# Optimization experiments

Hardware: AMD Instinct MI355X
Metric: run time of the kernel (lower is better)

Reference implementation:

```python
import jax, jax.numpy as jnp
import numpy as np

N = 200000   # graph nodes
C = 1000     # virtual nodes (clusters)
D = 256      # feature dim (in = hidden = out for this layer)


def setup_inputs() -> dict:
    key = jax.random.key(0)
    ks = jax.random.split(key, 24)
    W = lambda k, shape: jax.random.normal(k, shape, dtype=jnp.float32) * 0.05
    inp = {
        "h": jax.random.normal(ks[0], (N, D), dtype=jnp.float32),
        "g": jax.random.normal(ks[1], (C, D), dtype=jnp.float32),
        "g_hat": jax.random.normal(ks[2], (C, D), dtype=jnp.float32),
        "node2cluster": jax.random.randint(ks[3], (N,), 0, C),
        # AdditiveAttention params (all hidden_dim=D)
        "Wq": W(ks[4], (D, D)),          # query_proj (no bias)
        "Wk": W(ks[5], (D, D)),          # key_proj (no bias)
        "b_attn": jax.random.uniform(ks[6], (D,), jnp.float32, -0.1, 0.1),
        "w_score": W(ks[7], (D,)),       # score_proj weight (D -> 1)
        "b_score": jnp.zeros((), jnp.float32),
        # VNTransmitterUnit.W (D -> D), activation tanh
        "Wv": W(ks[8], (D, D)), "bv": jnp.zeros((D,), jnp.float32),
        # GNTransmitterUnit.F_super (D -> D), tanh
        "Ws": W(ks[9], (D, D)), "bs": jnp.zeros((D,), jnp.float32),
        # gn_merge WarpGateUnit (graph-node side)
        "H1w": W(ks[10], (D, D)), "H1b": jnp.zeros((D,), jnp.float32),
        "G1w": W(ks[11], (D, D)), "G1b": jnp.zeros((D,), jnp.float32),
        # vn_merge WarpGateUnit (virtual-node side)
        "H2w": W(ks[12], (D, D)), "H2b": jnp.zeros((D,), jnp.float32),
        "G2w": W(ks[13], (D, D)), "G2b": jnp.zeros((D,), jnp.float32),
    }
    return inp


def reference(h, g, g_hat, node2cluster,
              Wq, Wk, b_attn, w_score, b_score, Wv, bv, Ws, bs,
              H1w, H1b, G1w, G1b, H2w, H2b, G2w, G2b):
    seg = node2cluster  # (N,) cluster id of each node (the code's vn_index partition)

    # ---- VNTransmitterUnit: segmented additive (Bahdanau) attention, graph -> virtual ----
    # score_proj(tanh(key_proj(cluster_h) + query_proj(g[c]) + bias))
    q = g @ Wq                                             # (C, D)
    k = h @ Wk                                             # (N, D)
    s = jnp.tanh(k + q[seg] + b_attn) @ w_score + b_score  # (N,) per-node score
    # online per-cluster softmax (replaces Python loop over clusters)
    m = jax.ops.segment_max(s, seg, num_segments=C)        # (C,)
    e = jnp.exp(s - m[seg])                                # (N,)
    denom = jax.ops.segment_sum(e, seg, num_segments=C)    # (C,)
    attn = e / denom[seg]                                  # (N,)
    ctx = jax.ops.segment_sum(attn[:, None] * h, seg, num_segments=C)  # (C, D)
    g_trans = jnp.tanh(ctx @ Wv + bv)                      # VNTransmitter: W + tanh

    # ---- GNTransmitterUnit: virtual -> graph, tanh(F_super(g)) then per-node gather ----
    h_trans = jnp.tanh(g @ Ws + bs)                        # (C, D)
    h_trans_n = h_trans[seg]                               # (N, D) index_select by vn_indices[:,1]

    # ---- gn_merge WarpGateUnit: gated fuse on graph nodes ----
    z1 = jax.nn.sigmoid(h @ H1w + H1b + h_trans_n @ G1w + G1b)  # (N, D)
    h_merged = (1.0 - z1) * h + z1 * h_trans_n                   # (N, D)

    # ---- vn_merge WarpGateUnit: gated fuse on virtual nodes (g_hat = vn_update conv out) ----
    z2 = jax.nn.sigmoid(g_trans @ H2w + H2b + g_hat @ G2w + G2b)  # (C, D)
    vx_new = (1.0 - z2) * g_trans + z2 * g_hat                    # (C, D)

    # concat node-side and virtual-side outputs along rows -> (N + C, D)
    return jnp.concatenate([h_merged, vx_new], axis=0)
```

## Files before the change

kernel.cpp:

```cpp
#include <hip/hip_runtime.h>
#include <hip/hip_bf16.h>

#define Nn 200000
#define Cc 1000
#define Dd 256
#define PAD 16
#define NCH8 3125
#define CAP 512

typedef float f32x16 __attribute__((ext_vector_type(16)));
typedef short bf16x8 __attribute__((ext_vector_type(8)));
typedef _Float16 f16x2 __attribute__((ext_vector_type(2)));

#define LOG2E  1.4426950408889634f
#define LOG2E2 2.8853900817779268f

__device__ __forceinline__ unsigned int f2bf(float x){
    union { float f; unsigned int u; } c; c.f = x;
    unsigned int u = c.u;
    u += 0x7fffu + ((u >> 16) & 1u);
    return u >> 16;
}
__device__ __forceinline__ float bf2f(unsigned short b){
    union { unsigned int u; float f; } c; c.u = ((unsigned int)b) << 16;
    return c.f;
}
__device__ __forceinline__ float rcp_(float x){ return __builtin_amdgcn_rcpf(x); }

__global__ void k_prep(const float* __restrict__ Wk, const float* __restrict__ H1w,
                       unsigned short* __restrict__ wfragK, unsigned short* __restrict__ wfragH,
                       int* __restrict__ cnt){
    int t = blockIdx.x*256 + threadIdx.x;
    if (t < Cc*PAD) cnt[t] = 0;
    int arr = t >> 13;
    int s   = t & 8191;
    int ct  = s >> 10;
    int kk  = (s >> 6) & 15;
    int l   = s & 63;
    int col = ct*32 + (l & 31);
    int k0  = kk*16 + (l >> 5)*8;
    const float* W = arr ? H1w : Wk;
    unsigned short* dst = (arr ? wfragH : wfragK) + (size_t)s*8;
    #pragma unroll
    for (int e = 0; e < 8; ++e) dst[e] = (unsigned short)f2bf(W[(size_t)(k0+e)*Dd + col]);
}

__global__ __launch_bounds__(512)
void k_cluster_prep(const float* __restrict__ g, const float* __restrict__ Wq,
                    const float* __restrict__ b_attn,
                    const float* __restrict__ Ws, const float* __restrict__ bs,
                    const float* __restrict__ G1w, const float* __restrict__ G1b,
                    const float* __restrict__ H1b,
                    float* __restrict__ qb, unsigned int* __restrict__ ctht){
    int c = blockIdx.x, t = threadIdx.x;
    int d = t & 255, half = t >> 8;
    __shared__ float gL[Dd], htL[Dd];
    __shared__ float redA[2][Dd], redS[2][Dd];
    if (half == 0) gL[d] = g[(size_t)c*Dd + d];
    __syncthreads();
    int k0 = half*128;
    float aq = 0.f, as = 0.f;
    #pragma unroll 4
    for (int k2 = 0; k2 < 128; ++k2){
        int k = k0 + k2;
        float gv = gL[k];
        aq = fmaf(gv, Wq[k*Dd + d], aq);
        as = fmaf(gv, Ws[k*Dd + d], as);
    }
    redA[half][d] = aq;
    redS[half][d] = as;
    __syncthreads();
    if (half == 0){
        qb[(size_t)c*Dd + d] = redA[0][d] + redA[1][d] + b_attn[d];
        htL[d] = tanhf(redS[0][d] + redS[1][d] + bs[d]);
    }
    __syncthreads();
    float ac = 0.f;
    #pragma unroll 4
    for (int k2 = 0; k2 < 128; ++k2){
        int k = k0 + k2;
        ac = fmaf(htL[k], G1w[k*Dd + d], ac);
    }
    redA[half][d] = ac;
    __syncthreads();
    if (half == 0){
        float acv = redA[0][d] + redA[1][d] + H1b[d] + G1b[d];
        ctht[(size_t)c*Dd + d] = (f2bf(acv) << 16) | f2bf(htL[d]);
    }
}

__global__ void k_scatter(const int* __restrict__ seg, int* __restrict__ cnt, int* __restrict__ order){
    int i = blockIdx.x*256 + threadIdx.x;
    if (i < Nn){
        int c = seg[i];
        int p = atomicAdd(&cnt[c*PAD], 1);
        if (p < CAP) order[c*CAP + p] = i;
    }
}

__global__ __launch_bounds__(1024, 4)
void k_gemm8(const float* __restrict__ h, const unsigned short* __restrict__ wfrag,
             const int* __restrict__ seg, const float* __restrict__ qb,
             const float* __restrict__ w_score, const float* __restrict__ b_score,
             const unsigned int* __restrict__ ctht,
             float* __restrict__ e, float* __restrict__ out){
    __shared__ __align__(16) char Al[32768];
    __shared__ float sPart[64][8];
    __shared__ int segL[64];

    int tid = threadIdx.x;
    int w = tid >> 6, l = tid & 63;
    int lCol = l & 31, hiK = l >> 5;
    int rowBase = blockIdx.x * 64;

    {
        const float4* hv = reinterpret_cast<const float4*>(h + (size_t)rowBase * Dd);
        float4 v[4];
        #pragma unroll
        for (int j = 0; j < 4; ++j) v[j] = hv[j*1024 + tid];
        if (tid < 64) segL[tid] = seg[rowBase + tid];
        #pragma unroll
        for (int j = 0; j < 4; ++j){
            int f = j*1024 + tid;
            int row = f >> 6;
            unsigned long long pk = (unsigned long long)f2bf(v[j].x)
                                  | ((unsigned long long)f2bf(v[j].y) << 16)
                                  | ((unsigned long long)f2bf(v[j].z) << 32)
                                  | ((unsigned long long)f2bf(v[j].w) << 48);
            int byte = (row*512 + (f & 63)*8) ^ ((row & 15) << 4);
            *reinterpret_cast<unsigned long long*>(Al + byte) = pk;
        }
    }
    __syncthreads();

    int hOff = lCol*512;
    int swzK = (lCol & 15) << 4;
    const char* wb = reinterpret_cast<const char*>(wfrag) + (size_t)w*16384 + l*16;

    f32x16 acc0, acc1;
    #pragma unroll
    for (int i = 0; i < 16; ++i){ acc0[i] = 0.f; acc1[i] = 0.f; }
    #pragma unroll
    for (int kk = 0; kk < 16; ++kk){
        bf16x8 wF = *reinterpret_cast<const bf16x8*>(wb + (size_t)kk*1024);
        int hb = (hOff + kk*32 + hiK*16) ^ swzK;
        bf16x8 hF0 = *reinterpret_cast<const bf16x8*>(Al + hb);
        bf16x8 hF1 = *reinterpret_cast<const bf16x8*>(Al + 16384 + hb);
        acc0 = __builtin_amdgcn_mfma_f32_32x32x16_bf16(hF0, wF, acc0, 0, 0, 0);
        acc1 = __builtin_amdgcn_mfma_f32_32x32x16_bf16(hF1, wF, acc1, 0, 0, 0);
    }

    if (w < 8){
        float wsc = w_score[w*32 + lCol];
        #pragma unroll
        for (int nt = 0; nt < 2; ++nt){
            const f32x16& A = nt ? acc1 : acc0;
            #pragma unroll
            for (int p = 0; p < 8; ++p){
                int i0 = 2*p, i1 = 2*p + 1;
                int n0 = nt*32 + (i0&3) + 8*(i0>>2) + 4*hiK;
                int n1 = nt*32 + (i1&3) + 8*(i1>>2) + 4*hiK;
                float q0 = qb[(size_t)segL[n0]*Dd + w*32 + lCol];
                float q1 = qb[(size_t)segL[n1]*Dd + w*32 + lCol];
                float t0 = exp2f(LOG2E2*(A[i0] + q0));
                float t1 = exp2f(LOG2E2*(A[i1] + q1));
                float v0 = (t0 - 1.f)*rcp_(t0 + 1.f)*wsc;
                float v1 = (t1 - 1.f)*rcp_(t1 + 1.f)*wsc;
                f16x2 pk; pk.x = (_Float16)v0; pk.y = (_Float16)v1;
                #pragma unroll
                for (int off = 1; off <= 16; off <<= 1){
                    union { f16x2 f; int i; } cv, co;
                    cv.f = pk;
                    co.i = __shfl_xor(cv.i, off);
                    pk = pk + co.f;
                }
                if (lCol == 0){
                    sPart[n0][w] = (float)pk.x;
                    sPart[n1][w] = (float)pk.y;
                }
            }
        }
    } else {
        int cb = (w - 8)*32 + lCol;
        #pragma unroll
        for (int nt = 0; nt < 2; ++nt){
            const f32x16& A = nt ? acc1 : acc0;
            #pragma unroll
            for (int i = 0; i < 16; ++i){
                int node = nt*32 + (i&3) + 8*(i>>2) + 4*hiK;
                unsigned int v = ctht[(size_t)segL[node]*Dd + cb];
                float c4 = bf2f((unsigned short)(v >> 16));
                float t4 = bf2f((unsigned short)(v & 0xffff));
                unsigned short hb = *reinterpret_cast<const unsigned short*>(
                    Al + ((node*512 + cb*2) ^ ((node & 15) << 4)));
                float hval = bf2f(hb);
                float z = rcp_(1.f + exp2f(-LOG2E*(A[i] + c4)));
                out[(size_t)(rowBase + node)*Dd + cb] = fmaf(z, t4 - hval, hval);
            }
        }
    }

    __syncthreads();
    if (tid < 64){
        float s = sPart[tid][0] + sPart[tid][1] + sPart[tid][2] + sPart[tid][3]
                + sPart[tid][4] + sPart[tid][5] + sPart[tid][6] + sPart[tid][7] + b_score[0];
        e[rowBase + tid] = exp2f(LOG2E * s);
    }
}

__global__ __launch_bounds__(512)
void k_ctx(const float* __restrict__ h, const float* __restrict__ e,
           const int* __restrict__ order, const int* __restrict__ cnt,
           float* __restrict__ ctxPart, float* __restrict__ denPart){
    int b = blockIdx.x;
    int c = b >> 3, q = b & 7;
    int n_all = min(cnt[c*PAD], CAP);
    int c0 = (n_all * q) >> 3, c1 = (n_all * (q+1)) >> 3;
    int n = c1 - c0;
    int start = c*CAP + c0;
    int t = threadIdx.x;
    __shared__ int idxL[512];
    __shared__ float eL[512];
    __shared__ float redL[8][256];
    __shared__ float dsum[8];
    int r8 = t >> 6;
    int col4 = (t & 63) << 2;
    float ax = 0.f, ay = 0.f, az = 0.f, aw = 0.f;
    float dpart = 0.f;
    for (int base = 0; base < n; base += 512){
        int m = min(512, n - base);
        if (t < m){
            int nd = order[start + base + t];
            idxL[t] = nd;
            float ev = e[nd];
            eL[t] = ev;
            dpart += ev;
        }
        __syncthreads();
        #pragma unroll 8
        for (int i = r8; i < m; i += 8){
            float ev = eL[i];
            float4 hv = *reinterpret_cast<const float4*>(h + (size_t)idxL[i]*Dd + col4);
            ax = fmaf(ev, hv.x, ax);
            ay = fmaf(ev, hv.y, ay);
            az = fmaf(ev, hv.z, az);
            aw = fmaf(ev, hv.w, aw);
        }
        __syncthreads();
    }
    *reinterpret_cast<float4*>(&redL[r8][col4]) = (float4){ax, ay, az, aw};
    #pragma unroll
    for (int off = 1; off < 64; off <<= 1) dpart += __shfl_xor(dpart, off);
    if ((t & 63) == 0) dsum[r8] = dpart;
    __syncthreads();
    if (t < 256){
        float s = ((redL[0][t] + redL[1][t]) + (redL[2][t] + redL[3][t]))
                + ((redL[4][t] + redL[5][t]) + (redL[6][t] + redL[7][t]));
        ctxPart[((size_t)c*8 + q)*Dd + t] = s;
    }
    if (t == 0)
        denPart[b] = ((dsum[0]+dsum[1])+(dsum[2]+dsum[3]))+((dsum[4]+dsum[5])+(dsum[6]+dsum[7]));
}

__global__ __launch_bounds__(512)
void k_vn(const float* __restrict__ ctxPart, const float* __restrict__ denPart,
          const float* __restrict__ g_hat,
          const float* __restrict__ Wv, const float* __restrict__ bv,
          const float* __restrict__ H2w, const float* __restrict__ H2b,
          const float* __restrict__ G2w, const float* __restrict__ G2b,
          float* __restrict__ out){
    int c = blockIdx.x, t = threadIdx.x;
    int d = t & 255, half = t >> 8;
    __shared__ float cL[Dd], gtL[Dd], ghL[Dd];
    __shared__ float red[2][Dd];
    if (half == 0){
        float den = 0.f, num = 0.f;
        #pragma unroll
        for (int q = 0; q < 8; ++q){
            den += denPart[c*8 + q];
            num += ctxPart[((size_t)c*8 + q)*Dd + d];
        }
        float inv = (den > 0.f) ? 1.f/den : 0.f;
        cL[d]  = num * inv;
        ghL[d] = g_hat[(size_t)c*Dd + d];
    }
    __syncthreads();
    int k0 = half*128;
    float a1 = 0.f;
    #pragma unroll 4
    for (int k2 = 0; k2 < 128; ++k2){
        int k = k0 + k2;
        a1 = fmaf(cL[k], Wv[k*Dd + d], a1);
    }
    red[half][d] = a1;
    __syncthreads();
    if (half == 0)
        gtL[d] = tanhf(red[0][d] + red[1][d] + bv[d]);
    __syncthreads();
    float a2 = 0.f;
    #pragma unroll 4
    for (int k2 = 0; k2 < 128; ++k2){
        int k = k0 + k2;
        a2 = fmaf(gtL[k], H2w[k*Dd + d], a2);
        a2 = fmaf(ghL[k], G2w[k*Dd + d], a2);
    }
    red[half][d] = a2;
    __syncthreads();
    if (half == 0){
        float a2v = red[0][d] + red[1][d] + H2b[d] + G2b[d];
        float z = 1.f / (1.f + expf(-a2v));
        out[(size_t)(Nn + c)*Dd + d] = (1.f - z)*gtL[d] + z*ghL[d];
    }
}

extern "C" void kernel_launch(void* const* d_in, const int* in_sizes, int n_in,
                              void* d_out, int out_size, void* d_ws, size_t ws_size,
                              hipStream_t stream){
    const float* h       = (const float*)d_in[0];
    const float* g       = (const float*)d_in[1];
    const float* g_hat   = (const float*)d_in[2];
    const int*   seg     = (const int*)  d_in[3];
    const float* Wq      = (const float*)d_in[4];
    const float* Wk      = (const float*)d_in[5];
    const float* b_attn  = (const float*)d_in[6];
    const float* w_score = (const float*)d_in[7];
    const float* b_score = (const float*)d_in[8];
    const float* Wv      = (const float*)d_in[9];
    const float* bv      = (const float*)d_in[10];
    const float* Ws      = (const float*)d_in[11];
    const float* bs      = (const float*)d_in[12];
    const float* H1w     = (const float*)d_in[13];
    const float* H1b     = (const float*)d_in[14];
    const float* G1w     = (const float*)d_in[15];
    const float* G1b     = (const float*)d_in[16];
    const float* H2w     = (const float*)d_in[17];
    const float* H2b     = (const float*)d_in[18];
    const float* G2w     = (const float*)d_in[19];
    const float* G2b     = (const float*)d_in[20];
    float* out = (float*)d_out;

    char* ws = (char*)d_ws;
    unsigned short* wfragK = (unsigned short*)(ws + 0);
    unsigned short* wfragH = (unsigned short*)(ws + 131072);
    float* qb          = (float*)(ws +  262144);
    unsigned int* ctht = (unsigned int*)(ws + 1286144);
    float* e       = (float*)(ws + 2310144);
    int*   order   = (int*)  (ws + 3110144);
    int*   cnt     = (int*)  (ws + 5158144);
    float* ctxPart = (float*)(ws + 5222144);
    float* denPart = (float*)(ws + 13414144);

    hipLaunchKernelGGL(k_prep, dim3(64), dim3(256), 0, stream, Wk, H1w, wfragK, wfragH, cnt);
    hipLaunchKernelGGL(k_cluster_prep, dim3(Cc), dim3(512), 0, stream,
                       g, Wq, b_attn, Ws, bs, G1w, G1b, H1b, qb, ctht);
    hipLaunchKernelGGL(k_scatter, dim3((Nn + 255)/256), dim3(256), 0, stream, seg, cnt, order);
    hipLaunchKernelGGL(k_gemm8, dim3(NCH8), dim3(1024), 0, stream,
                       h, wfragK, seg, qb, w_score, b_score, ctht, e, out);
    hipLaunchKernelGGL(k_ctx, dim3(Cc*8), dim3(512), 0, stream, h, e, order, cnt, ctxPart, denPart);
    hipLaunchKernelGGL(k_vn, dim3(Cc), dim3(512), 0, stream,
                       ctxPart, denPart, g_hat, Wv, bv, H2w, H2b, G2w, G2b, out);
}
```

Before: 298.0 us.

## Halve gemm block to 512 threads, each wave computing score and gate tiles

The fused node GEMM kernel now runs 8 waves per block instead of 16. Each wave computes both the attention-score column tile and the matching gate column tile, so the shared-memory h fragments are read once per k-step for two MFMAs. The h-to-bf16 conversion also switches from manual rounding to the hardware v_cvt_pk_bf16_f32 packed instruction. This cuts LDS read traffic and conversion ALU work, but doubles the accumulator registers per wave and leaves fewer waves per block to hide latency.

```diff
diff --git a/kernel.cpp b/kernel.cpp
--- a/kernel.cpp
+++ b/kernel.cpp
@@ -26,6 +26,11 @@
     return c.f;
 }
 __device__ __forceinline__ float rcp_(float x){ return __builtin_amdgcn_rcpf(x); }
+__device__ __forceinline__ unsigned int cvtpk_bf16(float lo, float hi){
+    unsigned int r;
+    asm("v_cvt_pk_bf16_f32 %0, %1, %2" : "=v"(r) : "v"(lo), "v"(hi));
+    return r;
+}
 
 __global__ void k_prep(const float* __restrict__ Wk, const float* __restrict__ H1w,
                        unsigned short* __restrict__ wfragK, unsigned short* __restrict__ wfragH,
@@ -98,8 +103,8 @@
     }
 }
 
-__global__ __launch_bounds__(1024, 4)
-void k_gemm8(const float* __restrict__ h, const unsigned short* __restrict__ wfrag,
+__global__ __launch_bounds__(512, 4)
+void k_gemm9(const float* __restrict__ h, const unsigned short* __restrict__ wfrag,
              const int* __restrict__ seg, const float* __restrict__ qb,
              const float* __restrict__ w_score, const float* __restrict__ b_score,
              const unsigned int* __restrict__ ctht,
@@ -115,46 +120,49 @@
 
     {
         const float4* hv = reinterpret_cast<const float4*>(h + (size_t)rowBase * Dd);
-        float4 v[4];
-        #pragma unroll
-        for (int j = 0; j < 4; ++j) v[j] = hv[j*1024 + tid];
+        float4 v[8];
+        #pragma unroll
+        for (int j = 0; j < 8; ++j) v[j] = hv[j*512 + tid];
         if (tid < 64) segL[tid] = seg[rowBase + tid];
         #pragma unroll
-        for (int j = 0; j < 4; ++j){
-            int f = j*1024 + tid;
+        for (int j = 0; j < 8; ++j){
+            int f = j*512 + tid;
             int row = f >> 6;
-            unsigned long long pk = (unsigned long long)f2bf(v[j].x)
-                                  | ((unsigned long long)f2bf(v[j].y) << 16)
-                                  | ((unsigned long long)f2bf(v[j].z) << 32)
-                                  | ((unsigned long long)f2bf(v[j].w) << 48);
+            uint2 pk;
+            pk.x = cvtpk_bf16(v[j].x, v[j].y);
+            pk.y = cvtpk_bf16(v[j].z, v[j].w);
             int byte = (row*512 + (f & 63)*8) ^ ((row & 15) << 4);
-            *reinterpret_cast<unsigned long long*>(Al + byte) = pk;
+            *reinterpret_cast<uint2*>(Al + byte) = pk;
         }
     }
     __syncthreads();
 
     int hOff = lCol*512;
     int swzK = (lCol & 15) << 4;
-    const char* wb = reinterpret_cast<const char*>(wfrag) + (size_t)w*16384 + l*16;
-
-    f32x16 acc0, acc1;
+    const char* wbS = reinterpret_cast<const char*>(wfrag) + (size_t)w*16384     + l*16;
+    const char* wbM = reinterpret_cast<const char*>(wfrag) + (size_t)(w+8)*16384 + l*16;
+
+    f32x16 aS0, aS1, aM0, aM1;
     #pragma unroll
-    for (int i = 0; i < 16; ++i){ acc0[i] = 0.f; acc1[i] = 0.f; }
+    for (int i = 0; i < 16; ++i){ aS0[i] = 0.f; aS1[i] = 0.f; aM0[i] = 0.f; aM1[i] = 0.f; }
     #pragma unroll
     for (int kk = 0; kk < 16; ++kk){
-        bf16x8 wF = *reinterpret_cast<const bf16x8*>(wb + (size_t)kk*1024);
+        bf16x8 wFS = *reinterpret_cast<const bf16x8*>(wbS + (size_t)kk*1024);
+        bf16x8 wFM = *reinterpret_cast<const bf16x8*>(wbM + (size_t)kk*1024);
         int hb = (hOff + kk*32 + hiK*16) ^ swzK;
         bf16x8 hF0 = *reinterpret_cast<const bf16x8*>(Al + hb);
         bf16x8 hF1 = *reinterpret_cast<const bf16x8*>(Al + 16384 + hb);
-        acc0 = __builtin_amdgcn_mfma_f32_32x32x16_bf16(hF0, wF, acc0, 0, 0, 0);
-        acc1 = __builtin_amdgcn_mfma_f32_32x32x16_bf16(hF1, wF, acc1, 0, 0, 0);
-    }
-
-    if (w < 8){
+        aS0 = __builtin_amdgcn_mfma_f32_32x32x16_bf16(hF0, wFS, aS0, 0, 0, 0);
+        aS1 = __builtin_amdgcn_mfma_f32_32x32x16_bf16(hF1, wFS, aS1, 0, 0, 0);
+        aM0 = __builtin_amdgcn_mfma_f32_32x32x16_bf16(hF0, wFM, aM0, 0, 0, 0);
+        aM1 = __builtin_amdgcn_mfma_f32_32x32x16_bf16(hF1, wFM, aM1, 0, 0, 0);
+    }
+
+    {
         float wsc = w_score[w*32 + lCol];
         #pragma unroll
         for (int nt = 0; nt < 2; ++nt){
-            const f32x16& A = nt ? acc1 : acc0;
+            const f32x16& A = nt ? aS1 : aS0;
             #pragma unroll
             for (int p = 0; p < 8; ++p){
                 int i0 = 2*p, i1 = 2*p + 1;
@@ -180,11 +188,13 @@
                 }
             }
         }
-    } else {
-        int cb = (w - 8)*32 + lCol;
+    }
+
+    {
+        int cb = w*32 + lCol;
         #pragma unroll
         for (int nt = 0; nt < 2; ++nt){
-            const f32x16& A = nt ? acc1 : acc0;
+            const f32x16& A = nt ? aM1 : aM0;
             #pragma unroll
             for (int i = 0; i < 16; ++i){
                 int node = nt*32 + (i&3) + 8*(i>>2) + 4*hiK;
@@ -354,7 +364,7 @@
     hipLaunchKernelGGL(k_cluster_prep, dim3(Cc), dim3(512), 0, stream,
                        g, Wq, b_attn, Ws, bs, G1w, G1b, H1b, qb, ctht);
     hipLaunchKernelGGL(k_scatter, dim3((Nn + 255)/256), dim3(256), 0, stream, seg, cnt, order);
-    hipLaunchKernelGGL(k_gemm8, dim3(NCH8), dim3(1024), 0, stream,
+    hipLaunchKernelGGL(k_gemm9, dim3(NCH8), dim3(512), 0, stream,
                        h, wfragK, seg, qb, w_score, b_score, ctht, e, out);
     hipLaunchKernelGGL(k_ctx, dim3(Cc*8), dim3(512), 0, stream, h, e, order, cnt, ctxPart, denPart);
     hipLaunchKernelGGL(k_vn, dim3(Cc), dim3(512), 0, stream,
```

After: 476.1 us. 1.6x slower.
